# Performance work log

Measured on AMD Instinct MI355X. Metric: run time of the kernel, lower is better.

## Reference

```python
import math
import jax, jax.numpy as jnp
import numpy as np

C = 1024
H = 8
EPS = 1e-5
SLOPE = 0.1


def _branch(x, W, gamma, beta, mean, var):
    # conv1x1 (no bias) -> BatchNorm1d (eval-mode stats) -> LeakyReLU(0.1)
    # x: [b, C, p], W: [C_out, C_in]
    y = jnp.einsum('oc,bcp->bop', W, x)
    scale = gamma / jnp.sqrt(var + EPS)          # [C]
    y = y * scale[:, None] + (beta - mean * scale)[:, None]
    return jnp.where(y > 0, y, SLOPE * y)


def setup_inputs() -> dict:
    key = jax.random.key(0)
    ks = jax.random.split(key, 20)
    b, pq, pk = 4, 2048, 2048
    d = {
        'Xq': jax.random.normal(ks[0], (b, C, pq), dtype=jnp.float32),
        'Xk': jax.random.normal(ks[1], (b, C, pk), dtype=jnp.float32),
        'Wq': jax.random.normal(ks[2], (C, C), dtype=jnp.float32) * (1.0 / math.sqrt(C)),
        'Wk': jax.random.normal(ks[3], (C, C), dtype=jnp.float32) * (1.0 / math.sqrt(C)),
        'Wv': jax.random.normal(ks[4], (C, C), dtype=jnp.float32) * (1.0 / math.sqrt(C)),
    }
    for i, tag in enumerate(['1', '2', '3']):
        d['gamma' + tag] = jnp.ones((C,), jnp.float32) + 0.1 * jax.random.normal(ks[5 + 4 * i], (C,), jnp.float32)
        d['beta' + tag] = 0.1 * jax.random.normal(ks[6 + 4 * i], (C,), jnp.float32)
        d['mean' + tag] = 0.1 * jax.random.normal(ks[7 + 4 * i], (C,), jnp.float32)
        d['var' + tag] = 0.5 + jax.random.uniform(ks[8 + 4 * i], (C,), jnp.float32)
    return d


def reference(Xq, Xk, Wq, Wk, Wv,
              gamma1, beta1, mean1, var1,
              gamma2, beta2, mean2, var2,
              gamma3, beta3, mean3, var3):
    Q = _branch(Xq, Wq, gamma1, beta1, mean1, var1)   # [b, C, pq]
    K = _branch(Xk, Wk, gamma2, beta2, mean2, var2)   # [b, C, pk]
    V = _branch(Xq, Wv, gamma3, beta3, mean3, var3)   # [b, C, pq]
    b, c, pk = K.shape
    pq = V.shape[-1]
    dh = c // H
    Qh = Q.reshape(b, H, dh, pq)
    Kh = K.reshape(b, H, dh, pk)
    Vh = V.reshape(b, H, dh, pq)
    # scores over channel dim: [b, h, pk, pq]
    Hmat = jnp.einsum('bhci,bhcj->bhij', Kh, Vh) / math.sqrt(c / H)
    Hmat = jax.nn.softmax(Hmat, axis=-1)
    out = jnp.einsum('bhij,bhcj->bhci', Hmat, Qh)     # [b, h, dh, pk]
    return out.reshape(b, c, pk)
```

## Files before the change

kernel.cpp:

```cpp
#include <hip/hip_runtime.h>

typedef __bf16 bf16_t;
typedef __bf16 bf16x8 __attribute__((ext_vector_type(8)));
typedef __bf16 bf16x4 __attribute__((ext_vector_type(4)));
typedef float  f32x4  __attribute__((ext_vector_type(4)));

#define WB_OFF  0LL
#define XQT_OFF 3145728LL
#define XKT_OFF 11534336LL
#define Q_OFF   19922944LL
#define KT_OFF  28311552LL
#define VT_OFF  36700160LL

__device__ __forceinline__ void gl_lds16(const bf16_t* g, bf16_t* l) {
  __builtin_amdgcn_global_load_lds((const __attribute__((address_space(1))) void*)(g),
                                   (__attribute__((address_space(3))) void*)(l), 16, 0, 0);
}

__device__ __forceinline__ bf16x4 cvt4(f32x4 v) {
  bf16x4 r;
  r[0] = (bf16_t)v[0]; r[1] = (bf16_t)v[1]; r[2] = (bf16_t)v[2]; r[3] = (bf16_t)v[3];
  return r;
}

__global__ __launch_bounds__(256) void k_wconv(
    const float* __restrict__ Wq, const float* __restrict__ Wk, const float* __restrict__ Wv,
    bf16_t* __restrict__ ws)
{
  const float* W = blockIdx.y == 0 ? Wq : (blockIdx.y == 1 ? Wk : Wv);
  bf16_t* dst = ws + WB_OFF + (long)blockIdx.y * 1048576;
  const long i = ((long)blockIdx.x * 256 + threadIdx.x) * 4;
  *(bf16x4*)&dst[i] = cvt4(*(const f32x4*)(W + i));
}

__global__ __launch_bounds__(256) void k_transpose(
    const float* __restrict__ Xq, const float* __restrict__ Xk, bf16_t* __restrict__ ws)
{
  __shared__ __align__(16) bf16_t t[64 * 72];
  const int z = blockIdx.z, b = z & 3, ts = z >> 2;
  const float* X = ts ? Xk : Xq;
  bf16_t* XT = ws + (ts ? XKT_OFF : XQT_OFF);
  const int p0 = blockIdx.x * 64, c0 = blockIdx.y * 64;
  const int tid = threadIdx.x;
  const int tx = tid & 15, ty = tid >> 4;
  const float* src = X + ((long)b * 1024 + c0) * 2048 + p0;
  #pragma unroll
  for (int hh = 0; hh < 4; ++hh) {
    int c = ty + hh * 16;
    f32x4 v = *(const f32x4*)(src + (long)c * 2048 + tx * 4);
    *(bf16x4*)&t[c * 72 + tx * 4] = cvt4(v);
  }
  __syncthreads();
  bf16_t* dst = XT + ((long)b * 2048 + p0) * 1024 + c0;
  #pragma unroll
  for (int hh = 0; hh < 2; ++hh) {
    int p = (tid >> 3) + hh * 32;
    int cc = tid & 7;
    bf16x8 v;
    #pragma unroll
    for (int j = 0; j < 8; ++j) v[j] = t[(cc * 8 + j) * 72 + p];
    *(bf16x8*)(dst + (long)p * 1024 + cc * 8) = v;
  }
}

__global__ __launch_bounds__(256) void k_qkv(
    const float* __restrict__ g1, const float* __restrict__ b1, const float* __restrict__ m1, const float* __restrict__ v1,
    const float* __restrict__ g2, const float* __restrict__ b2, const float* __restrict__ m2, const float* __restrict__ v2,
    const float* __restrict__ g3, const float* __restrict__ b3, const float* __restrict__ m3, const float* __restrict__ v3,
    bf16_t* __restrict__ ws)
{
  __shared__ __align__(16) bf16_t smem[17408];
  bf16_t* sa = smem;
  bf16_t* sb = smem + 8192;
  bf16_t* ep = smem;
  __shared__ float sS[128], sBi[128];

  const int tid = threadIdx.x;
  const int z = blockIdx.z, br = z >> 2, b = z & 3;
  const int o0 = blockIdx.y * 128, p0 = blockIdx.x * 128;

  const float *gm, *bt, *mn, *vr;
  const bf16_t *XT;
  bf16_t* dst;
  int tr;
  if (br == 0)      { XT = ws + XQT_OFF; gm = g1; bt = b1; mn = m1; vr = v1; dst = ws + Q_OFF;  tr = 0; }
  else if (br == 1) { XT = ws + XKT_OFF; gm = g2; bt = b2; mn = m2; vr = v2; dst = ws + KT_OFF; tr = 1; }
  else              { XT = ws + XQT_OFF; gm = g3; bt = b3; mn = m3; vr = v3; dst = ws + VT_OFF; tr = 1; }
  const bf16_t* W = ws + WB_OFF + (long)br * 1048576;

  if (tid < 128) {
    float g = gm[o0 + tid], be = bt[o0 + tid];
    float m = mn[o0 + tid], v = vr[o0 + tid];
    float sc = g / sqrtf(v + 1e-5f);
    sS[tid] = sc; sBi[tid] = be - m * sc;
  }

  const int w = tid >> 6, lane = tid & 63, quad = lane >> 4, l15 = lane & 15;
  const int wr = (w >> 1) * 64, wc = (w & 1) * 64;

  f32x4 acc[4][4];
  #pragma unroll
  for (int i = 0; i < 4; ++i)
    #pragma unroll
    for (int j = 0; j < 4; ++j) acc[i][j] = f32x4{0.f, 0.f, 0.f, 0.f};

  const bf16_t* Wb = W + (long)o0 * 1024;
  const bf16_t* Xb = XT + ((long)b * 2048 + p0) * 1024;

  for (int kk = 0; kk < 16; ++kk) {
    __syncthreads();
    const int kof = kk * 64;
    #pragma unroll
    for (int is = 0; is < 4; ++is) {
      int s = (is * 4 + w) * 64 + lane;
      int row = s >> 3, ch = s & 7;
      int col = kof + ((ch ^ (row & 7)) << 3);
      gl_lds16(Wb + (long)row * 1024 + col, &sa[(is * 4 + w) * 512]);
      gl_lds16(Xb + (long)row * 1024 + col, &sb[(is * 4 + w) * 512]);
    }
    __syncthreads();
    #pragma unroll
    for (int ks = 0; ks < 2; ++ks) {
      bf16x8 af[4], bfr[4];
      #pragma unroll
      for (int i = 0; i < 4; ++i) {
        int mm = wr + i * 16 + l15;
        af[i] = *(const bf16x8*)&sa[mm * 64 + (((ks * 4 + quad) ^ (mm & 7)) << 3)];
        int nn = wc + i * 16 + l15;
        bfr[i] = *(const bf16x8*)&sb[nn * 64 + (((ks * 4 + quad) ^ (nn & 7)) << 3)];
      }
      #pragma unroll
      for (int i = 0; i < 4; ++i)
        #pragma unroll
        for (int j = 0; j < 4; ++j)
          acc[i][j] = __builtin_amdgcn_mfma_f32_16x16x32_bf16(af[i], bfr[j], acc[i][j], 0, 0, 0);
    }
  }

  __syncthreads();
  #pragma unroll
  for (int i = 0; i < 4; ++i) {
    #pragma unroll
    for (int j = 0; j < 4; ++j) {
      const int p_l = wc + j * 16 + l15;
      const int ob = wr + i * 16 + quad * 4;
      if (!tr) {
        #pragma unroll
        for (int r = 0; r < 4; ++r) {
          float v = fmaf(acc[i][j][r], sS[ob + r], sBi[ob + r]);
          v = v > 0.f ? v : 0.1f * v;
          ep[(ob + r) * 136 + p_l] = (bf16_t)v;
        }
      } else {
        bf16x4 t4;
        #pragma unroll
        for (int r = 0; r < 4; ++r) {
          float v = fmaf(acc[i][j][r], sS[ob + r], sBi[ob + r]);
          v = v > 0.f ? v : 0.1f * v;
          t4[r] = (bf16_t)v;
        }
        *(bf16x4*)&ep[p_l * 136 + ob] = t4;
      }
    }
  }
  __syncthreads();
  #pragma unroll
  for (int pass = 0; pass < 8; ++pass) {
    int row = pass * 16 + (tid >> 4);
    int ch = tid & 15;
    bf16x8 v = *(const bf16x8*)&ep[row * 136 + ch * 8];
    long off;
    if (!tr) off = ((long)b * 1024 + o0 + row) * 2048 + p0 + ch * 8;
    else     off = ((long)b * 2048 + p0 + row) * 1024 + o0 + ch * 8;
    *(bf16x8*)&dst[off] = v;
  }
}

__global__ __launch_bounds__(512) void k_attn(const bf16_t* __restrict__ ws, float* __restrict__ out)
{
  __shared__ __align__(16) bf16_t sK[16384];
  __shared__ __align__(16) bf16_t sV[16384];
  __shared__ __align__(16) bf16_t sQ[16384];
  __shared__ __align__(16) bf16_t sP[16384];

  const int tid = threadIdx.x, w = tid >> 6, lane = tid & 63, quad = lane >> 4, l15 = lane & 15;
  const int i0 = blockIdx.x * 128, h = blockIdx.y, b = blockIdx.z;

  const bf16_t* KTb = ws + KT_OFF + ((long)b * 2048 + i0) * 1024 + h * 128;
  const bf16_t* VTb = ws + VT_OFF + ((long)b * 2048) * 1024 + h * 128;
  const bf16_t* Qb  = ws + Q_OFF  + ((long)b * 1024 + h * 128) * 2048;

  #pragma unroll
  for (int is = 0; is < 4; ++is) {
    int s = (is * 8 + w) * 64 + lane;
    int row = s >> 4, ch = s & 15;
    gl_lds16(KTb + (long)row * 1024 + ((ch ^ (row & 15)) << 3), &sK[(is * 8 + w) * 512]);
  }

  f32x4 U[8];
  #pragma unroll
  for (int f = 0; f < 8; ++f) U[f] = f32x4{0.f, 0.f, 0.f, 0.f};
  float ls[4] = {0.f, 0.f, 0.f, 0.f};

  const int irow = w * 16 + l15;
  const float SCL = 1.4426950408889634f * 0.08838834764831843f;

  for (int jt = 0; jt < 16; ++jt) {
    const int j0 = jt * 128;
    #pragma unroll
    for (int is = 0; is < 4; ++is) {
      int s = (is * 8 + w) * 64 + lane;
      int row = s >> 4, ch = s & 15;
      gl_lds16(VTb + (long)(j0 + row) * 1024 + ((ch ^ (row & 15)) << 3), &sV[(is * 8 + w) * 512]);
      gl_lds16(Qb + (long)row * 2048 + j0 + ((ch ^ (row & 15)) << 3), &sQ[(is * 8 + w) * 512]);
    }
    __syncthreads();

    bf16x8 af[4];
    #pragma unroll
    for (int ks = 0; ks < 4; ++ks)
      af[ks] = *(const bf16x8*)&sK[irow * 128 + (((ks * 4 + quad) ^ l15) << 3)];

    #pragma unroll
    for (int fj = 0; fj < 8; ++fj) {
      f32x4 S = f32x4{0.f, 0.f, 0.f, 0.f};
      const int jr = fj * 16 + l15;
      #pragma unroll
      for (int ks = 0; ks < 4; ++ks) {
        bf16x8 bfr = *(const bf16x8*)&sV[jr * 128 + (((ks * 4 + quad) ^ l15) << 3)];
        S = __builtin_amdgcn_mfma_f32_16x16x32_bf16(af[ks], bfr, S, 0, 0, 0);
      }
      #pragma unroll
      for (int r = 0; r < 4; ++r) {
        float p = exp2f(S[r] * SCL);
        ls[r] += p;
        const int il = w * 16 + quad * 4 + r;
        const int jl = fj * 16 + l15;
        sP[il * 128 + (((jl >> 3) ^ (il & 15)) << 3) + (jl & 7)] = (bf16_t)p;
      }
    }

    bf16x8 pf[4];
    #pragma unroll
    for (int ks = 0; ks < 4; ++ks)
      pf[ks] = *(const bf16x8*)&sP[irow * 128 + (((ks * 4 + quad) ^ l15) << 3)];

    #pragma unroll
    for (int fc = 0; fc < 8; ++fc) {
      const int cr = fc * 16 + l15;
      #pragma unroll
      for (int ks = 0; ks < 4; ++ks) {
        bf16x8 qf = *(const bf16x8*)&sQ[cr * 128 + (((ks * 4 + quad) ^ l15) << 3)];
        U[fc] = __builtin_amdgcn_mfma_f32_16x16x32_bf16(pf[ks], qf, U[fc], 0, 0, 0);
      }
    }
    __syncthreads();
  }

  #pragma unroll
  for (int r = 0; r < 4; ++r) {
    #pragma unroll
    for (int off = 1; off < 16; off <<= 1)
      ls[r] += __shfl_xor(ls[r], off, 64);
  }
  float rls[4];
  #pragma unroll
  for (int r = 0; r < 4; ++r) rls[r] = 1.0f / ls[r];

  #pragma unroll
  for (int fc = 0; fc < 8; ++fc) {
    const int c = h * 128 + fc * 16 + l15;
    f32x4 v;
    #pragma unroll
    for (int r = 0; r < 4; ++r) v[r] = U[fc][r] * rls[r];
    const long o = ((long)b * 1024 + c) * 2048 + i0 + w * 16 + quad * 4;
    *(f32x4*)&out[o] = v;
  }
}

extern "C" void kernel_launch(void* const* d_in, const int* in_sizes, int n_in,
                              void* d_out, int out_size, void* d_ws, size_t ws_size,
                              hipStream_t stream)
{
  (void)in_sizes; (void)n_in; (void)out_size; (void)ws_size;
  const float* Xq = (const float*)d_in[0];
  const float* Xk = (const float*)d_in[1];
  const float* Wq = (const float*)d_in[2];
  const float* Wk = (const float*)d_in[3];
  const float* Wv = (const float*)d_in[4];
  bf16_t* ws = (bf16_t*)d_ws;
  float* out = (float*)d_out;

  k_wconv<<<dim3(1024, 3), 256, 0, stream>>>(Wq, Wk, Wv, ws);
  k_transpose<<<dim3(32, 16, 8), 256, 0, stream>>>(Xq, Xk, ws);
  k_qkv<<<dim3(16, 8, 12), 256, 0, stream>>>(
      (const float*)d_in[5],  (const float*)d_in[6],  (const float*)d_in[7],  (const float*)d_in[8],
      (const float*)d_in[9],  (const float*)d_in[10], (const float*)d_in[11], (const float*)d_in[12],
      (const float*)d_in[13], (const float*)d_in[14], (const float*)d_in[15], (const float*)d_in[16],
      ws);
  k_attn<<<dim3(16, 8, 4), 512, 0, stream>>>(ws, out);
}
```

Baseline: 336.8 us.

## Double-buffer V/Q tiles with smaller j-tiles and keep K fragments in registers

The attention kernel now splits the j dimension into 64-wide tiles and double-buffers the V and Q tiles in LDS, prefetching the next tile while computing the current one. K fragments are loaded straight from global memory into registers instead of staged through LDS, and the S MFMA operands are swapped so each lane holds a full row-sum and writes P as bf16x4 vectors. LDS use drops from 128KB to 80KB, and the launch bounds ask for a minimum of 4 waves per EU. The gains aimed for are overlap of global loads with MFMA work and better occupancy, at the cost of twice as many barriers per row block and more register pressure.

```diff
diff --git a/kernel.cpp b/kernel.cpp
--- a/kernel.cpp
+++ b/kernel.cpp
@@ -176,12 +176,11 @@
   }
 }
 
-__global__ __launch_bounds__(512) void k_attn(const bf16_t* __restrict__ ws, float* __restrict__ out)
-{
-  __shared__ __align__(16) bf16_t sK[16384];
-  __shared__ __align__(16) bf16_t sV[16384];
-  __shared__ __align__(16) bf16_t sQ[16384];
-  __shared__ __align__(16) bf16_t sP[16384];
+__global__ __launch_bounds__(512, 4) void k_attn(const bf16_t* __restrict__ ws, float* __restrict__ out)
+{
+  __shared__ __align__(16) bf16_t sV[2][8192];
+  __shared__ __align__(16) bf16_t sQ[2][8192];
+  __shared__ __align__(16) bf16_t sP[8192];
 
   const int tid = threadIdx.x, w = tid >> 6, lane = tid & 63, quad = lane >> 4, l15 = lane & 15;
   const int i0 = blockIdx.x * 128, h = blockIdx.y, b = blockIdx.z;
@@ -190,89 +189,92 @@
   const bf16_t* VTb = ws + VT_OFF + ((long)b * 2048) * 1024 + h * 128;
   const bf16_t* Qb  = ws + Q_OFF  + ((long)b * 1024 + h * 128) * 2048;
 
-  #pragma unroll
-  for (int is = 0; is < 4; ++is) {
-    int s = (is * 8 + w) * 64 + lane;
-    int row = s >> 4, ch = s & 15;
-    gl_lds16(KTb + (long)row * 1024 + ((ch ^ (row & 15)) << 3), &sK[(is * 8 + w) * 512]);
-  }
+  const int irow = w * 16 + l15;
+
+  bf16x8 af[4];
+  #pragma unroll
+  for (int ks = 0; ks < 4; ++ks)
+    af[ks] = *(const bf16x8*)(KTb + (long)irow * 1024 + (ks * 4 + quad) * 8);
 
   f32x4 U[8];
   #pragma unroll
   for (int f = 0; f < 8; ++f) U[f] = f32x4{0.f, 0.f, 0.f, 0.f};
-  float ls[4] = {0.f, 0.f, 0.f, 0.f};
-
-  const int irow = w * 16 + l15;
+  float ls = 0.f;
+
   const float SCL = 1.4426950408889634f * 0.08838834764831843f;
 
-  for (int jt = 0; jt < 16; ++jt) {
-    const int j0 = jt * 128;
-    #pragma unroll
-    for (int is = 0; is < 4; ++is) {
-      int s = (is * 8 + w) * 64 + lane;
-      int row = s >> 4, ch = s & 15;
-      gl_lds16(VTb + (long)(j0 + row) * 1024 + ((ch ^ (row & 15)) << 3), &sV[(is * 8 + w) * 512]);
-      gl_lds16(Qb + (long)row * 2048 + j0 + ((ch ^ (row & 15)) << 3), &sQ[(is * 8 + w) * 512]);
-    }
-    __syncthreads();
-
-    bf16x8 af[4];
-    #pragma unroll
-    for (int ks = 0; ks < 4; ++ks)
-      af[ks] = *(const bf16x8*)&sK[irow * 128 + (((ks * 4 + quad) ^ l15) << 3)];
-
-    #pragma unroll
-    for (int fj = 0; fj < 8; ++fj) {
+  #define STAGE(jt, bb)                                                               \
+    {                                                                                 \
+      const int j0_ = (jt) * 64;                                                      \
+      _Pragma("unroll")                                                               \
+      for (int rnd = 0; rnd < 2; ++rnd) {                                             \
+        int s = rnd * 512 + tid;                                                      \
+        int vrow = s >> 4, vch = s & 15;                                              \
+        gl_lds16(VTb + (long)(j0_ + vrow) * 1024 + ((vch ^ (vrow & 15)) << 3),        \
+                 &sV[bb][s * 8]);                                                     \
+        int qrow = s >> 3, qch = s & 7;                                               \
+        gl_lds16(Qb + (long)qrow * 2048 + j0_ + ((qch ^ (qrow & 7)) << 3),            \
+                 &sQ[bb][s * 8]);                                                     \
+      }                                                                               \
+    }
+
+  STAGE(0, 0);
+  __syncthreads();
+
+  for (int jt = 0; jt < 32; ++jt) {
+    const int cur = jt & 1;
+    if (jt < 31) STAGE(jt + 1, cur ^ 1);
+
+    #pragma unroll
+    for (int fj = 0; fj < 4; ++fj) {
       f32x4 S = f32x4{0.f, 0.f, 0.f, 0.f};
       const int jr = fj * 16 + l15;
       #pragma unroll
       for (int ks = 0; ks < 4; ++ks) {
-        bf16x8 bfr = *(const bf16x8*)&sV[jr * 128 + (((ks * 4 + quad) ^ l15) << 3)];
-        S = __builtin_amdgcn_mfma_f32_16x16x32_bf16(af[ks], bfr, S, 0, 0, 0);
-      }
+        bf16x8 vfr = *(const bf16x8*)&sV[cur][jr * 128 + (((ks * 4 + quad) ^ (jr & 15)) << 3)];
+        S = __builtin_amdgcn_mfma_f32_16x16x32_bf16(vfr, af[ks], S, 0, 0, 0);
+      }
+      bf16x4 p4;
       #pragma unroll
       for (int r = 0; r < 4; ++r) {
         float p = exp2f(S[r] * SCL);
-        ls[r] += p;
-        const int il = w * 16 + quad * 4 + r;
-        const int jl = fj * 16 + l15;
-        sP[il * 128 + (((jl >> 3) ^ (il & 15)) << 3) + (jl & 7)] = (bf16_t)p;
-      }
-    }
-
-    bf16x8 pf[4];
-    #pragma unroll
-    for (int ks = 0; ks < 4; ++ks)
-      pf[ks] = *(const bf16x8*)&sP[irow * 128 + (((ks * 4 + quad) ^ l15) << 3)];
+        ls += p;
+        p4[r] = (bf16_t)p;
+      }
+      const int i = w * 16 + l15;
+      const int jl = fj * 16 + quad * 4;
+      *(bf16x4*)&sP[i * 64 + (((jl >> 3) ^ (i & 7)) << 3) + (jl & 7)] = p4;
+    }
+
+    bf16x8 pf[2];
+    #pragma unroll
+    for (int ks = 0; ks < 2; ++ks)
+      pf[ks] = *(const bf16x8*)&sP[irow * 64 + (((ks * 4 + quad) ^ (irow & 7)) << 3)];
 
     #pragma unroll
     for (int fc = 0; fc < 8; ++fc) {
-      const int cr = fc * 16 + l15;
-      #pragma unroll
-      for (int ks = 0; ks < 4; ++ks) {
-        bf16x8 qf = *(const bf16x8*)&sQ[cr * 128 + (((ks * 4 + quad) ^ l15) << 3)];
+      const int c = fc * 16 + l15;
+      #pragma unroll
+      for (int ks = 0; ks < 2; ++ks) {
+        bf16x8 qf = *(const bf16x8*)&sQ[cur][c * 64 + (((ks * 4 + quad) ^ (c & 7)) << 3)];
         U[fc] = __builtin_amdgcn_mfma_f32_16x16x32_bf16(pf[ks], qf, U[fc], 0, 0, 0);
       }
     }
     __syncthreads();
   }
 
-  #pragma unroll
-  for (int r = 0; r < 4; ++r) {
-    #pragma unroll
-    for (int off = 1; off < 16; off <<= 1)
-      ls[r] += __shfl_xor(ls[r], off, 64);
-  }
-  float rls[4];
-  #pragma unroll
-  for (int r = 0; r < 4; ++r) rls[r] = 1.0f / ls[r];
+  ls += __shfl_xor(ls, 16, 64);
+  ls += __shfl_xor(ls, 32, 64);
+  float* lsum = (float*)&sP[(w * 16) * 64];
+  if (quad == 0) lsum[l15] = ls;
+  f32x4 rl4 = *(const f32x4*)&lsum[quad * 4];
 
   #pragma unroll
   for (int fc = 0; fc < 8; ++fc) {
     const int c = h * 128 + fc * 16 + l15;
     f32x4 v;
     #pragma unroll
-    for (int r = 0; r < 4; ++r) v[r] = U[fc][r] * rls[r];
+    for (int r = 0; r < 4; ++r) v[r] = U[fc][r] / rl4[r];
     const long o = ((long)b * 1024 + c) * 2048 + i0 + w * 16 + quad * 4;
     *(f32x4*)&out[o] = v;
   }
```

Result: faster. 292.1 us (-13.3%).
